# Kernel optimization log

Hardware: AMD Instinct MI355X
Metric: run time of the kernel (lower is better)

The kernel has to match this reference:

```python
import jax, jax.numpy as jnp
import numpy as np

# FP8 E4M3 pulse encoder constants (from init_kwargs defaults)
E_BITS = 4
M_BITS = 3
N_INT = 10          # scan_integer_bits
N_DEC = 10          # scan_decimal_bits
TOTAL_STEPS = N_INT + N_DEC
BIAS = 2 ** (E_BITS - 1) - 1        # 7
START_EXP = N_INT + BIAS            # down-counter start value (17)
SUB_START = N_INT + 6               # subnormal window start (== N_INT + BIAS - 1)


def setup_inputs() -> dict:
    key = jax.random.key(0)
    x = jax.random.normal(key, (8, 2048, 1024), dtype=jnp.float32)
    return {"x": x}


def _encode(x):
    dt = x.dtype
    shp = x.shape
    xf = x.reshape(-1)                      # [n]
    s_out = (xf < 0).astype(dt)             # sign bit (inhibitory SignBitNode)
    abs_x = jnp.abs(xf)
    n = xf.shape[0]

    def step(carry, t):
        V, has_fired, d, e_reg, m_reg = carry
        # DynamicThresholdIFNode: soft-reset IF, threshold 2^(N_INT-1-t)
        thr = jnp.exp2((N_INT - 1 - t).astype(dt))
        s = (V >= thr).astype(dt)
        V = V - s * thr
        # first-spike detection: fs = s AND NOT(has_fired)
        fs = s * (1.0 - has_fired)
        active = (t < SUB_START).astype(dt)  # scalar gate for normal-range latching
        # TemporalExponentGenerator: down-counter, LSB-first bits
        counter = jnp.maximum(START_EXP - 1 - t, 0)
        exp_bits = ((counter >> jnp.arange(E_BITS)) & 1).astype(dt)   # [E]
        # latch exponent at first spike (VecAND + VecOR accumulate)
        e_reg = jnp.maximum(e_reg, exp_bits[None, :] * (fs * active)[:, None])
        # delay line: d[:, i] holds fs(t-1-i); sample mantissa bits with current s
        m_reg = jnp.maximum(m_reg, s[:, None] * d)
        valid_fs = fs * active
        d = jnp.concatenate([valid_fs[:, None], d[:, :-1]], axis=1)
        # accumulate has_fired only during normal window
        has_fired = jnp.maximum(has_fired, fs * active)
        # subnormal window: directly sample m_reg[t - SUB_START] when never fired
        onehot = (jnp.arange(M_BITS) == (t - SUB_START)).astype(dt)   # [M]
        m_reg = jnp.maximum(m_reg, onehot[None, :] * (s * (1.0 - has_fired))[:, None])
        return (V, has_fired, d, e_reg, m_reg), None

    init = (abs_x,
            jnp.zeros((n,), dt),
            jnp.zeros((n, M_BITS), dt),
            jnp.zeros((n, E_BITS), dt),
            jnp.zeros((n, M_BITS), dt))
    (_, _, _, e_reg, m_reg), _ = jax.lax.scan(step, init, jnp.arange(TOTAL_STEPS))

    e_out = e_reg[:, ::-1]                   # LSB-first -> MSB-first (flip)
    out = jnp.concatenate([s_out[:, None], e_out, m_reg], axis=-1)
    return out.reshape(shp + (1 + E_BITS + M_BITS,))


def reference(x):
    return _encode(x)
```

## Files before the change

### kernel.cpp

```cpp
#include <hip/hip_runtime.h>


typedef float f32x4 __attribute__((ext_vector_type(4)));

__device__ __forceinline__ void encode_one(float x, f32x4& lo, f32x4& hi) {
    float sign = (x < 0.0f) ? 1.0f : 0.0f;
    unsigned ub = __float_as_uint(x) & 0x7fffffffu;
    float a = __uint_as_float(ub);
    int e_lead = (int)(ub >> 23) - 127;

    int ec, mant;
    if (__builtin_expect(e_lead >= 10, 0)) {
        float V = a;
        int has_fired = 0, d0 = 0, d1 = 0, d2 = 0;
        int e_reg = 0, m0 = 0, m1 = 0, m2 = 0;
        for (int t = 0; t < 20; ++t) {
            float thr = __builtin_exp2f((float)(9 - t));
            int s = (V >= thr) ? 1 : 0;
            if (s) V -= thr;
            int fs = s & (has_fired ^ 1);
            int active = (t < 16) ? 1 : 0;
            int counter = (16 - t) > 0 ? (16 - t) : 0;
            if (fs & active) e_reg |= (counter & 15);
            if (s) { m0 |= d0; m1 |= d1; m2 |= d2; }
            int vfs = fs & active;
            d2 = d1; d1 = d0; d0 = vfs;
            has_fired |= vfs;
            if (t >= 16 && t <= 18) {
                int bit = s & (has_fired ^ 1);
                if (t == 16) m0 |= bit; else if (t == 17) m1 |= bit; else m2 |= bit;
            }
        }
        ec = e_reg;
        mant = (m0 << 2) | (m1 << 1) | m2;
    } else {
        bool norm = (e_lead >= -6);
        bool sub  = (e_lead >= -10) & !norm;
        int ec_n   = (7 + e_lead) & 15;
        int mant_n = (int)(ub >> 20) & 7;
        int mant_s = ((int)(a * 512.0f)) & 7;
        ec   = norm ? ec_n : 0;
        mant = norm ? mant_n : (sub ? mant_s : 0);
    }

    lo.x = sign;
    lo.y = (float)((ec >> 3) & 1);
    lo.z = (float)((ec >> 2) & 1);
    lo.w = (float)((ec >> 1) & 1);
    hi.x = (float)(ec & 1);
    hi.y = (float)((mant >> 2) & 1);
    hi.z = (float)((mant >> 1) & 1);
    hi.w = (float)(mant & 1);
}

__global__ __launch_bounds__(256) void pulse_encode_kernel(
        const f32x4* __restrict__ in4, f32x4* __restrict__ out4) {
    __shared__ f32x4 lds[2048];
    const int t = threadIdx.x;
    const int blk = blockIdx.x;

    f32x4 v = __builtin_nontemporal_load(&in4[blk * 256 + t]);

    f32x4 lo0, hi0, lo1, hi1, lo2, hi2, lo3, hi3;
    encode_one(v.x, lo0, hi0);
    encode_one(v.y, lo1, hi1);
    encode_one(v.z, lo2, hi2);
    encode_one(v.w, lo3, hi3);

    const int base = t * 8;
    const int sw = t & 7;
    lds[(base + 0) ^ sw] = lo0;
    lds[(base + 1) ^ sw] = hi0;
    lds[(base + 2) ^ sw] = lo1;
    lds[(base + 3) ^ sw] = hi1;
    lds[(base + 4) ^ sw] = lo2;
    lds[(base + 5) ^ sw] = hi2;
    lds[(base + 6) ^ sw] = lo3;
    lds[(base + 7) ^ sw] = hi3;

    __syncthreads();

    const int obase = blk * 2048;
    const int rsw = (t >> 3) & 7;
#pragma unroll
    for (int k = 0; k < 8; ++k) {
        int s = t + 256 * k;
        f32x4 val = lds[s ^ rsw];
        __builtin_nontemporal_store(val, &out4[obase + s]);
    }
}

__global__ __launch_bounds__(256) void pulse_encode_tail(
        const float* __restrict__ in, f32x4* __restrict__ out, int n) {
    int i = blockIdx.x * 256 + threadIdx.x;
    if (i >= n) return;
    f32x4 lo, hi;
    encode_one(in[i], lo, hi);
    out[2 * i]     = lo;
    out[2 * i + 1] = hi;
}

extern "C" void kernel_launch(void* const* d_in, const int* in_sizes, int n_in,
                              void* d_out, int out_size, void* d_ws, size_t ws_size,
                              hipStream_t stream) {
    const float* x = (const float*)d_in[0];
    f32x4* out = (f32x4*)d_out;
    int n = in_sizes[0];
    int nblocks = n / 1024;
    if (nblocks > 0) {
        pulse_encode_kernel<<<nblocks, 256, 0, stream>>>(
            (const f32x4*)x, out);
    }
    int done = nblocks * 1024;
    int rem = n - done;
    if (rem > 0) {
        int tb = (rem + 255) / 256;
        pulse_encode_tail<<<tb, 256, 0, stream>>>(x + done, out + 2 * done, rem);
    }
}
```

Baseline: 552.4 us.

## Use persistent grid-stride blocks with next-tile prefetch and plain loads/stores

Replaces the one-tile-per-block launch with at most 2048 persistent blocks that loop over tiles. Each iteration prefetches the next tile's input before encoding the current one, which is meant to overlap load latency with compute and LDS transposition and to cut block launch overhead. It also drops the nontemporal load/store builtins in favour of ordinary accesses, and adds a second barrier per iteration so the LDS buffer can be reused safely.

```diff
diff --git a/kernel.cpp b/kernel.cpp
--- a/kernel.cpp
+++ b/kernel.cpp
@@ -54,39 +54,50 @@
 }
 
 __global__ __launch_bounds__(256) void pulse_encode_kernel(
-        const f32x4* __restrict__ in4, f32x4* __restrict__ out4) {
+        const f32x4* __restrict__ in4, f32x4* __restrict__ out4, int ntiles) {
     __shared__ f32x4 lds[2048];
     const int t = threadIdx.x;
-    const int blk = blockIdx.x;
+    const int stride = gridDim.x;
+    int tile = blockIdx.x;
+    if (tile >= ntiles) return;
 
-    f32x4 v = __builtin_nontemporal_load(&in4[blk * 256 + t]);
+    f32x4 v = in4[tile * 256 + t];
 
-    f32x4 lo0, hi0, lo1, hi1, lo2, hi2, lo3, hi3;
-    encode_one(v.x, lo0, hi0);
-    encode_one(v.y, lo1, hi1);
-    encode_one(v.z, lo2, hi2);
-    encode_one(v.w, lo3, hi3);
+    while (true) {
+        const int next = tile + stride;
+        f32x4 vn = v;
+        if (next < ntiles) vn = in4[next * 256 + t];
 
-    const int base = t * 8;
-    const int sw = t & 7;
-    lds[(base + 0) ^ sw] = lo0;
-    lds[(base + 1) ^ sw] = hi0;
-    lds[(base + 2) ^ sw] = lo1;
-    lds[(base + 3) ^ sw] = hi1;
-    lds[(base + 4) ^ sw] = lo2;
-    lds[(base + 5) ^ sw] = hi2;
-    lds[(base + 6) ^ sw] = lo3;
-    lds[(base + 7) ^ sw] = hi3;
+        f32x4 lo0, hi0, lo1, hi1, lo2, hi2, lo3, hi3;
+        encode_one(v.x, lo0, hi0);
+        encode_one(v.y, lo1, hi1);
+        encode_one(v.z, lo2, hi2);
+        encode_one(v.w, lo3, hi3);
 
-    __syncthreads();
+        __syncthreads();
+        const int base = t * 8;
+        const int sw = t & 7;
+        lds[(base + 0) ^ sw] = lo0;
+        lds[(base + 1) ^ sw] = hi0;
+        lds[(base + 2) ^ sw] = lo1;
+        lds[(base + 3) ^ sw] = hi1;
+        lds[(base + 4) ^ sw] = lo2;
+        lds[(base + 5) ^ sw] = hi2;
+        lds[(base + 6) ^ sw] = lo3;
+        lds[(base + 7) ^ sw] = hi3;
+        __syncthreads();
 
-    const int obase = blk * 2048;
-    const int rsw = (t >> 3) & 7;
+        const int obase = tile * 2048;
+        const int rsw = (t >> 3) & 7;
 #pragma unroll
-    for (int k = 0; k < 8; ++k) {
-        int s = t + 256 * k;
-        f32x4 val = lds[s ^ rsw];
-        __builtin_nontemporal_store(val, &out4[obase + s]);
+        for (int k = 0; k < 8; ++k) {
+            int s = t + 256 * k;
+            out4[obase + s] = lds[s ^ rsw];
+        }
+
+        if (next >= ntiles) break;
+        v = vn;
+        tile = next;
     }
 }
 
@@ -106,12 +117,13 @@
     const float* x = (const float*)d_in[0];
     f32x4* out = (f32x4*)d_out;
     int n = in_sizes[0];
-    int nblocks = n / 1024;
-    if (nblocks > 0) {
+    int ntiles = n / 1024;
+    if (ntiles > 0) {
+        int nblocks = ntiles < 2048 ? ntiles : 2048;
         pulse_encode_kernel<<<nblocks, 256, 0, stream>>>(
-            (const f32x4*)x, out);
+            (const f32x4*)x, out, ntiles);
     }
-    int done = nblocks * 1024;
+    int done = ntiles * 1024;
     int rem = n - done;
     if (rem > 0) {
         int tb = (rem + 255) / 256;
```

Result: no change. 563.0 us (+1.9%).
